# Kernel tuning notes

Measured on AMD Instinct MI355X. Metric: run time of the kernel, lower is better.

## Reference

```python
import jax, jax.numpy as jnp
import numpy as np

EPSILON_BASE = 0.1
N_ITERS = 10


def setup_inputs() -> dict:
    key = jax.random.key(0)
    k1, k2 = jax.random.split(key)
    N, D = 8192, 512
    embeddings = jax.random.normal(k1, (N, D), dtype=jnp.float32)
    target_noise = jax.random.normal(k2, (N, D), dtype=jnp.float32)
    return {"embeddings": embeddings, "target_noise": target_noise}


def _l2_normalize(x, axis=1, eps=1e-12):
    # matches torch.nn.functional.normalize (divide by max(norm, eps))
    norm = jnp.sqrt(jnp.sum(x * x, axis=axis, keepdims=True))
    return x / jnp.maximum(norm, eps)


def _sinkhorn(x, y):
    n, d = x.shape
    # normalize_embeddings=True path
    x = _l2_normalize(x, axis=1)
    y = _l2_normalize(y, axis=1)
    epsilon = EPSILON_BASE * 2.0
    # squared euclidean cost: C[i,j] = ||x_i - y_j||^2  (cdist p=2, squared)
    sq_x = jnp.sum(x * x, axis=1, keepdims=True)          # (n,1)
    sq_y = jnp.sum(y * y, axis=1, keepdims=True)          # (n,1)
    C = jnp.maximum(sq_x + sq_y.T - 2.0 * (x @ y.T), 0.0)  # (n,n)
    log_K = -C / epsilon

    def body(carry, _):
        log_u, log_v = carry
        log_u = -jax.nn.logsumexp(log_K + log_v[None, :], axis=1)
        log_v = -jax.nn.logsumexp(log_K.T + log_u[None, :], axis=1)
        return (log_u, log_v), None

    init = (jnp.zeros(n, dtype=x.dtype), jnp.zeros(n, dtype=y.dtype))
    (log_u, log_v), _ = jax.lax.scan(body, init, None, length=N_ITERS)

    log_P = log_u[:, None] + log_K + log_v[None, :]
    P = jnp.clip(jnp.exp(log_P), 0.0, 1.0)
    distance = jnp.sum(P * C) / n

    # nan/inf fallback: 1 - mean cosine similarity (x, y already unit norm)
    fallback = 1.0 - jnp.mean(jnp.sum(x * y, axis=1))
    bad = jnp.isnan(distance) | jnp.isinf(distance)
    return jnp.where(bad, fallback, distance)


def reference(embeddings, target_noise):
    if embeddings.ndim == 3:
        embeddings = embeddings.reshape(-1, embeddings.shape[-1])
        target_noise = target_noise.reshape(-1, target_noise.shape[-1])
    return _sinkhorn(embeddings, target_noise)
```

## Files before the change

kernel.cpp:

```cpp
#include <hip/hip_runtime.h>
#include <hip/hip_bf16.h>
#include <hip/hip_fp16.h>
#include <stdint.h>

#define NROW 8192
#define DIM  512
#define LN2   0.6931471805599453f
#define TEN_LOG2E 14.426950408889634f

typedef __attribute__((ext_vector_type(8))) short short8;
typedef __attribute__((ext_vector_type(4))) float f32x4;
typedef __attribute__((ext_vector_type(2))) float f32x2;

__device__ __forceinline__ float block_sum256(float v) {
  #pragma unroll
  for (int off = 32; off > 0; off >>= 1) v += __shfl_down(v, off, 64);
  __shared__ float sb[4];
  const int w = threadIdx.x >> 6;
  if ((threadIdx.x & 63) == 0) sb[w] = v;
  __syncthreads();
  return sb[0] + sb[1] + sb[2] + sb[3];
}

__global__ __launch_bounds__(256) void init_kernel(float* __restrict__ colrcp,
                                                   float* __restrict__ diagacc,
                                                   float* __restrict__ distacc) {
  const int g = blockIdx.x * 256 + threadIdx.x;
  colrcp[g] = 1.0f;
  if (g == 0) { diagacc[0] = 0.f; distacc[0] = 0.f; }
}

__global__ __launch_bounds__(256) void normalize_kernel(
    const float* __restrict__ X, const float* __restrict__ Y,
    __hip_bfloat16* __restrict__ Xn, __hip_bfloat16* __restrict__ Yn,
    float* __restrict__ diagacc) {
  const int wave = threadIdx.x >> 6, lane = threadIdx.x & 63;
  float dsum = 0.f;
  #pragma unroll
  for (int rr = 0; rr < 4; rr++) {
    const int row = blockIdx.x * 16 + wave * 4 + rr;
    const float4* xr = (const float4*)(X + (size_t)row * DIM);
    const float4* yr = (const float4*)(Y + (size_t)row * DIM);
    float4 x0 = xr[lane], x1 = xr[lane + 64];
    float4 y0 = yr[lane], y1 = yr[lane + 64];
    float sx = x0.x*x0.x + x0.y*x0.y + x0.z*x0.z + x0.w*x0.w
             + x1.x*x1.x + x1.y*x1.y + x1.z*x1.z + x1.w*x1.w;
    float sy = y0.x*y0.x + y0.y*y0.y + y0.z*y0.z + y0.w*y0.w
             + y1.x*y1.x + y1.y*y1.y + y1.z*y1.z + y1.w*y1.w;
    float sxy = x0.x*y0.x + x0.y*y0.y + x0.z*y0.z + x0.w*y0.w
              + x1.x*y1.x + x1.y*y1.y + x1.z*y1.z + x1.w*y1.w;
    #pragma unroll
    for (int off = 1; off < 64; off <<= 1) {
      sx  += __shfl_xor(sx, off, 64);
      sy  += __shfl_xor(sy, off, 64);
      sxy += __shfl_xor(sxy, off, 64);
    }
    const float rx = 1.0f / fmaxf(sqrtf(sx), 1e-12f);
    const float ry = 1.0f / fmaxf(sqrtf(sy), 1e-12f);
    if (lane == 0) dsum += sxy * rx * ry;
    ushort4 px, py;
    { __hip_bfloat16 b;
      b = __float2bfloat16(x0.x*rx); px.x = *(unsigned short*)&b;
      b = __float2bfloat16(x0.y*rx); px.y = *(unsigned short*)&b;
      b = __float2bfloat16(x0.z*rx); px.z = *(unsigned short*)&b;
      b = __float2bfloat16(x0.w*rx); px.w = *(unsigned short*)&b;
      b = __float2bfloat16(y0.x*ry); py.x = *(unsigned short*)&b;
      b = __float2bfloat16(y0.y*ry); py.y = *(unsigned short*)&b;
      b = __float2bfloat16(y0.z*ry); py.z = *(unsigned short*)&b;
      b = __float2bfloat16(y0.w*ry); py.w = *(unsigned short*)&b;
    }
    ((ushort4*)(Xn + (size_t)row * DIM))[lane] = px;
    ((ushort4*)(Yn + (size_t)row * DIM))[lane] = py;
    { __hip_bfloat16 b;
      b = __float2bfloat16(x1.x*rx); px.x = *(unsigned short*)&b;
      b = __float2bfloat16(x1.y*rx); px.y = *(unsigned short*)&b;
      b = __float2bfloat16(x1.z*rx); px.z = *(unsigned short*)&b;
      b = __float2bfloat16(x1.w*rx); px.w = *(unsigned short*)&b;
      b = __float2bfloat16(y1.x*ry); py.x = *(unsigned short*)&b;
      b = __float2bfloat16(y1.y*ry); py.y = *(unsigned short*)&b;
      b = __float2bfloat16(y1.z*ry); py.z = *(unsigned short*)&b;
      b = __float2bfloat16(y1.w*ry); py.w = *(unsigned short*)&b;
    }
    ((ushort4*)(Xn + (size_t)row * DIM))[lane + 64] = px;
    ((ushort4*)(Yn + (size_t)row * DIM))[lane + 64] = py;
  }
  if (lane == 0) atomicAdd(diagacc, dsum);
}

__global__ __launch_bounds__(256) void gemm_kernel(
    const __hip_bfloat16* __restrict__ A, const __hip_bfloat16* __restrict__ B,
    uint8_t* __restrict__ K, uint8_t* __restrict__ KT) {
  __shared__ short As[128 * 32];
  __shared__ short Bs[128 * 32];
  const int m0 = blockIdx.y * 128;
  const int n0 = blockIdx.x * 128;
  const int t = threadIdx.x;
  const int wave = t >> 6, lane = t & 63;
  const int wm = (wave & 1) * 64, wn = (wave >> 1) * 64;
  const int fr = lane & 15;
  const int fq = lane >> 4;

  f32x4 acc[4][4];
  #pragma unroll
  for (int i = 0; i < 4; i++)
    #pragma unroll
    for (int j = 0; j < 4; j++) acc[i][j] = (f32x4)0.f;

  const int L0 = t, L1 = t + 256;
  const int ar0 = L0 >> 2, ac0 = L0 & 3;
  const int ar1 = L1 >> 2, ac1 = L1 & 3;
  const int4* Ag = (const int4*)A;
  const int4* Bg = (const int4*)B;

  for (int kt = 0; kt < 16; ++kt) {
    const int kb = kt * 4;
    int4 a0 = Ag[(size_t)(m0 + ar0) * 64 + kb + ac0];
    int4 a1 = Ag[(size_t)(m0 + ar1) * 64 + kb + ac1];
    int4 b0 = Bg[(size_t)(n0 + ar0) * 64 + kb + ac0];
    int4 b1 = Bg[(size_t)(n0 + ar1) * 64 + kb + ac1];
    __syncthreads();
    ((int4*)As)[L0] = a0;
    ((int4*)As)[L1] = a1;
    ((int4*)Bs)[L0] = b0;
    ((int4*)Bs)[L1] = b1;
    __syncthreads();
    short8 af[4], bfr[4];
    #pragma unroll
    for (int i = 0; i < 4; i++) {
      af[i]  = *(const short8*)&As[(wm + i * 16 + fr) * 32 + fq * 8];
      bfr[i] = *(const short8*)&Bs[(wn + i * 16 + fr) * 32 + fq * 8];
    }
    #pragma unroll
    for (int i = 0; i < 4; i++)
      #pragma unroll
      for (int j = 0; j < 4; j++)
        acc[i][j] = __builtin_amdgcn_mfma_f32_16x16x32_bf16(af[i], bfr[j], acc[i][j], 0, 0, 0);
  }
  #pragma unroll
  for (int i = 0; i < 4; i++) {
    #pragma unroll
    for (int j = 0; j < 4; j++) {
      const int R  = wm + i * 16 + fq * 4;
      const int Cc = wn + j * 16 + fr;
      float v0 = exp2f(fminf(acc[i][j][0], 1.0f) * TEN_LOG2E);
      float v1 = exp2f(fminf(acc[i][j][1], 1.0f) * TEN_LOG2E);
      float v2 = exp2f(fminf(acc[i][j][2], 1.0f) * TEN_LOG2E);
      float v3 = exp2f(fminf(acc[i][j][3], 1.0f) * TEN_LOG2E);
      int pk = 0;
      pk = __builtin_amdgcn_cvt_pk_fp8_f32(v0, v1, pk, false);
      pk = __builtin_amdgcn_cvt_pk_fp8_f32(v2, v3, pk, true);
      *(int*)(KT + (size_t)(n0 + Cc) * NROW + m0 + R) = pk;
      uint8_t* kp = K + (size_t)(m0 + R) * NROW + n0 + Cc;
      kp[0]            = (uint8_t)(pk & 0xff);
      kp[NROW]         = (uint8_t)((pk >> 8) & 0xff);
      kp[2 * NROW]     = (uint8_t)((pk >> 16) & 0xff);
      kp[3 * NROW]     = (uint8_t)((pk >> 24) & 0xff);
    }
  }
}

__global__ __launch_bounds__(256) void pass_kernel(
    const uint8_t* __restrict__ M, const float* __restrict__ w,
    float* __restrict__ out) {
  __shared__ float4 wl[2048];
  const int t = threadIdx.x;
  #pragma unroll
  for (int c = 0; c < 8; c++) wl[c * 256 + t] = ((const float4*)w)[c * 256 + t];
  __syncthreads();
  const int wave = t >> 6, lane = t & 63;
  const int row = blockIdx.x * 4 + wave;
  const int4* Mr = (const int4*)(M + (size_t)row * NROW);
  int4 k[8];
  #pragma unroll
  for (int c = 0; c < 8; c++) k[c] = Mr[c * 64 + lane];
  float acc0 = 0.f, acc1 = 0.f;
  #pragma unroll
  for (int c = 0; c < 8; c++) {
    const int base = (c * 64 + lane) * 4;
    const int* kd = (const int*)&k[c];
    #pragma unroll
    for (int q = 0; q < 4; q++) {
      float4 ww = wl[base + q];
      f32x2 lo = __builtin_amdgcn_cvt_pk_f32_fp8(kd[q], false);
      f32x2 hi = __builtin_amdgcn_cvt_pk_f32_fp8(kd[q], true);
      acc0 += lo.x * ww.x + lo.y * ww.y;
      acc1 += hi.x * ww.z + hi.y * ww.w;
    }
  }
  float acc = acc0 + acc1;
  #pragma unroll
  for (int off = 32; off > 0; off >>= 1) acc += __shfl_down(acc, off, 64);
  if (lane == 0) out[row] = 1.0f / acc;
}

__global__ __launch_bounds__(256) void dist_kernel(
    const uint8_t* __restrict__ K, const float* __restrict__ v,
    const float* __restrict__ u, float* __restrict__ distacc) {
  __shared__ float4 wl[2048];
  const int t = threadIdx.x;
  #pragma unroll
  for (int c = 0; c < 8; c++) wl[c * 256 + t] = ((const float4*)v)[c * 256 + t];
  __syncthreads();
  const int wave = t >> 6, lane = t & 63;
  const int row = blockIdx.x * 4 + wave;
  const float ui = u[row];
  const int4* Kr = (const int4*)(K + (size_t)row * NROW);
  float acc = 0.f;
  #pragma unroll 2
  for (int c = 0; c < 8; c++) {
    int4 kq = Kr[c * 64 + lane];
    const int base = (c * 64 + lane) * 4;
    const int* kd = (const int*)&kq;
    #pragma unroll
    for (int q = 0; q < 4; q++) {
      float4 ww = wl[base + q];
      f32x2 lo = __builtin_amdgcn_cvt_pk_f32_fp8(kd[q], false);
      f32x2 hi = __builtin_amdgcn_cvt_pk_f32_fp8(kd[q], true);
      float kv[4] = {lo.x, lo.y, hi.x, hi.y};
      float wv[4] = {ww.x, ww.y, ww.z, ww.w};
      #pragma unroll
      for (int e = 0; e < 4; e++) {
        float p = fminf(ui * kv[e] * wv[e], 1.f);
        float cterm = 2.f - 0.2f * LN2 * __log2f(fmaxf(kv[e], 1e-6f));
        acc += p * cterm;
      }
    }
  }
  float tot = block_sum256(acc);
  if (t == 0) atomicAdd(distacc, tot);
}

__global__ void final_kernel(const float* __restrict__ distacc,
                             const float* __restrict__ diagacc,
                             float* __restrict__ out) {
  if (threadIdx.x == 0 && blockIdx.x == 0) {
    float d = distacc[0] * (1.0f / (float)NROW);
    float fb = 1.0f - diagacc[0] * (1.0f / (float)NROW);
    float v = (isnan(d) || isinf(d)) ? fb : d;
    __hip_bfloat16 b = __float2bfloat16(v);
    unsigned short h = *(unsigned short*)&b;
    ((unsigned int*)out)[0] = ((unsigned int)h << 16) | (unsigned int)h;
  }
}

extern "C" void kernel_launch(void* const* d_in, const int* in_sizes, int n_in,
                              void* d_out, int out_size, void* d_ws, size_t ws_size,
                              hipStream_t stream) {
  (void)in_sizes; (void)n_in; (void)out_size; (void)ws_size;
  const float* X = (const float*)d_in[0];
  const float* Y = (const float*)d_in[1];
  float* out = (float*)d_out;

  char* ws = (char*)d_ws;
  size_t off = 0;
  uint8_t* K  = (uint8_t*)(ws + off); off += (size_t)NROW * NROW;
  uint8_t* KT = (uint8_t*)(ws + off); off += (size_t)NROW * NROW;
  __hip_bfloat16* Xn = (__hip_bfloat16*)(ws + off); off += (size_t)NROW * DIM * 2;
  __hip_bfloat16* Yn = (__hip_bfloat16*)(ws + off); off += (size_t)NROW * DIM * 2;
  float* rowrcp  = (float*)(ws + off); off += NROW * 4;
  float* colrcp  = (float*)(ws + off); off += NROW * 4;
  float* diagacc = (float*)(ws + off); off += 256;
  float* distacc = (float*)(ws + off); off += 256;

  init_kernel<<<32, 256, 0, stream>>>(colrcp, diagacc, distacc);
  normalize_kernel<<<512, 256, 0, stream>>>(X, Y, Xn, Yn, diagacc);
  gemm_kernel<<<dim3(64, 64), 256, 0, stream>>>(Xn, Yn, K, KT);
  for (int it = 0; it < 10; ++it) {
    pass_kernel<<<2048, 256, 0, stream>>>(K,  colrcp, rowrcp);
    pass_kernel<<<2048, 256, 0, stream>>>(KT, rowrcp, colrcp);
  }
  dist_kernel<<<2048, 256, 0, stream>>>(K, colrcp, rowrcp, distacc);
  final_kernel<<<1, 64, 0, stream>>>(distacc, diagacc, out);
}
```

Before: 500.2 us.

## Fuse final column pass into distance kernel and restage GEMM transposed stores

The tenth column-scaling pass is folded into the distance kernel, which works over the transposed matrix. It computes v per row in registers and then sums P*C, so one full pass over the 64MB fp8 matrix is dropped. The GEMM epilogue now builds the row-major K tile through shared memory and writes it with coalesced 16-byte stores, replacing scattered byte stores. The LDS layouts for the GEMM operands and the weight vectors get XOR swizzles to avoid bank conflicts. The pass kernels also handle two rows per wave, so each LDS weight load feeds two rows.

Result: slower. 526.5 us (+5.3%).

```diff
diff --git a/kernel.cpp b/kernel.cpp
--- a/kernel.cpp
+++ b/kernel.cpp
@@ -1,6 +1,5 @@
 #include <hip/hip_runtime.h>
 #include <hip/hip_bf16.h>
-#include <hip/hip_fp16.h>
 #include <stdint.h>
 
 #define NROW 8192
@@ -12,21 +11,17 @@
 typedef __attribute__((ext_vector_type(4))) float f32x4;
 typedef __attribute__((ext_vector_type(2))) float f32x2;
 
-__device__ __forceinline__ float block_sum256(float v) {
-  #pragma unroll
-  for (int off = 32; off > 0; off >>= 1) v += __shfl_down(v, off, 64);
-  __shared__ float sb[4];
-  const int w = threadIdx.x >> 6;
-  if ((threadIdx.x & 63) == 0) sb[w] = v;
-  __syncthreads();
-  return sb[0] + sb[1] + sb[2] + sb[3];
-}
-
-__global__ __launch_bounds__(256) void init_kernel(float* __restrict__ colrcp,
+__device__ __forceinline__ float dot4fp8(int pk, float4 w) {
+  f32x2 lo = __builtin_amdgcn_cvt_pk_f32_fp8(pk, false);
+  f32x2 hi = __builtin_amdgcn_cvt_pk_f32_fp8(pk, true);
+  return lo.x * w.x + lo.y * w.y + hi.x * w.z + hi.y * w.w;
+}
+
+__global__ __launch_bounds__(256) void init_kernel(float* __restrict__ v,
                                                    float* __restrict__ diagacc,
                                                    float* __restrict__ distacc) {
   const int g = blockIdx.x * 256 + threadIdx.x;
-  colrcp[g] = 1.0f;
+  v[g] = 1.0f;
   if (g == 0) { diagacc[0] = 0.f; distacc[0] = 0.f; }
 }
 
@@ -89,9 +84,12 @@
 
 __global__ __launch_bounds__(256) void gemm_kernel(
     const __hip_bfloat16* __restrict__ A, const __hip_bfloat16* __restrict__ B,
-    uint8_t* __restrict__ K, uint8_t* __restrict__ KT) {
-  __shared__ short As[128 * 32];
-  __shared__ short Bs[128 * 32];
+    uint8_t* __restrict__ Kmat, uint8_t* __restrict__ T) {
+  __shared__ __align__(16) char smem[16896];
+  int4* As4 = (int4*)smem;
+  int4* Bs4 = (int4*)(smem + 8192);
+  int*  tileT = (int*)smem;
+
   const int m0 = blockIdx.y * 128;
   const int n0 = blockIdx.x * 128;
   const int t = threadIdx.x;
@@ -106,29 +104,31 @@
     #pragma unroll
     for (int j = 0; j < 4; j++) acc[i][j] = (f32x4)0.f;
 
-  const int L0 = t, L1 = t + 256;
-  const int ar0 = L0 >> 2, ac0 = L0 & 3;
-  const int ar1 = L1 >> 2, ac1 = L1 & 3;
+  const int r0 = t >> 2, c0 = t & 3;
+  const int ph = c0 ^ ((r0 >> 2) & 3);
+  const int dst0 = r0 * 4 + ph;
+  const int dst1 = (64 + r0) * 4 + ph;
+  const int pc = fq ^ ((fr >> 2) & 3);
   const int4* Ag = (const int4*)A;
   const int4* Bg = (const int4*)B;
 
   for (int kt = 0; kt < 16; ++kt) {
     const int kb = kt * 4;
-    int4 a0 = Ag[(size_t)(m0 + ar0) * 64 + kb + ac0];
-    int4 a1 = Ag[(size_t)(m0 + ar1) * 64 + kb + ac1];
-    int4 b0 = Bg[(size_t)(n0 + ar0) * 64 + kb + ac0];
-    int4 b1 = Bg[(size_t)(n0 + ar1) * 64 + kb + ac1];
+    int4 a0 = Ag[(size_t)(m0 + r0) * 64 + kb + c0];
+    int4 a1 = Ag[(size_t)(m0 + 64 + r0) * 64 + kb + c0];
+    int4 b0 = Bg[(size_t)(n0 + r0) * 64 + kb + c0];
+    int4 b1 = Bg[(size_t)(n0 + 64 + r0) * 64 + kb + c0];
     __syncthreads();
-    ((int4*)As)[L0] = a0;
-    ((int4*)As)[L1] = a1;
-    ((int4*)Bs)[L0] = b0;
-    ((int4*)Bs)[L1] = b1;
+    As4[dst0] = a0;
+    As4[dst1] = a1;
+    Bs4[dst0] = b0;
+    Bs4[dst1] = b1;
     __syncthreads();
     short8 af[4], bfr[4];
     #pragma unroll
     for (int i = 0; i < 4; i++) {
-      af[i]  = *(const short8*)&As[(wm + i * 16 + fr) * 32 + fq * 8];
-      bfr[i] = *(const short8*)&Bs[(wn + i * 16 + fr) * 32 + fq * 8];
+      af[i]  = *(const short8*)&As4[(wm + i * 16 + fr) * 4 + pc];
+      bfr[i] = *(const short8*)&Bs4[(wn + i * 16 + fr) * 4 + pc];
     }
     #pragma unroll
     for (int i = 0; i < 4; i++)
@@ -136,12 +136,15 @@
       for (int j = 0; j < 4; j++)
         acc[i][j] = __builtin_amdgcn_mfma_f32_16x16x32_bf16(af[i], bfr[j], acc[i][j], 0, 0, 0);
   }
-  #pragma unroll
-  for (int i = 0; i < 4; i++) {
-    #pragma unroll
-    for (int j = 0; j < 4; j++) {
+  __syncthreads();
+  #pragma unroll
+  for (int j = 0; j < 4; j++) {
+    const int Cc = wn + j * 16 + fr;
+    uint8_t* Trow = T + (size_t)(n0 + Cc) * NROW + m0;
+    #pragma unroll
+    for (int i = 0; i < 4; i++) {
       const int R  = wm + i * 16 + fq * 4;
-      const int Cc = wn + j * 16 + fr;
+      const int Rq = (wm >> 2) + i * 4 + fq;
       float v0 = exp2f(fminf(acc[i][j][0], 1.0f) * TEN_LOG2E);
       float v1 = exp2f(fminf(acc[i][j][1], 1.0f) * TEN_LOG2E);
       float v2 = exp2f(fminf(acc[i][j][2], 1.0f) * TEN_LOG2E);
@@ -149,85 +152,167 @@
       int pk = 0;
       pk = __builtin_amdgcn_cvt_pk_fp8_f32(v0, v1, pk, false);
       pk = __builtin_amdgcn_cvt_pk_fp8_f32(v2, v3, pk, true);
-      *(int*)(KT + (size_t)(n0 + Cc) * NROW + m0 + R) = pk;
-      uint8_t* kp = K + (size_t)(m0 + R) * NROW + n0 + Cc;
-      kp[0]            = (uint8_t)(pk & 0xff);
-      kp[NROW]         = (uint8_t)((pk >> 8) & 0xff);
-      kp[2 * NROW]     = (uint8_t)((pk >> 16) & 0xff);
-      kp[3 * NROW]     = (uint8_t)((pk >> 24) & 0xff);
-    }
-  }
-}
-
-__global__ __launch_bounds__(256) void pass_kernel(
+      *(int*)(Trow + R) = pk;
+      tileT[Rq * 132 + Cc] = pk;
+    }
+  }
+  __syncthreads();
+  const int rl = t >> 1;
+  const int half = t & 1;
+  const int rq = rl >> 2;
+  const int rb = (rl & 3) * 8;
+  uint8_t* Krow = Kmat + (size_t)(m0 + rl) * NROW + n0 + half * 64;
+  #pragma unroll
+  for (int q = 0; q < 4; q++) {
+    const int base = rq * 132 + half * 64 + q * 16;
+    int4 w0 = *(const int4*)&tileT[base];
+    int4 w1 = *(const int4*)&tileT[base + 4];
+    int4 w2 = *(const int4*)&tileT[base + 8];
+    int4 w3 = *(const int4*)&tileT[base + 12];
+    int outv[4];
+    const int* wp[4] = {(const int*)&w0, (const int*)&w1, (const int*)&w2, (const int*)&w3};
+    #pragma unroll
+    for (int d = 0; d < 4; d++) {
+      const unsigned a0 = ((unsigned)wp[d][0] >> rb) & 0xffu;
+      const unsigned a1 = ((unsigned)wp[d][1] >> rb) & 0xffu;
+      const unsigned a2 = ((unsigned)wp[d][2] >> rb) & 0xffu;
+      const unsigned a3 = ((unsigned)wp[d][3] >> rb) & 0xffu;
+      outv[d] = (int)(a0 | (a1 << 8) | (a2 << 16) | (a3 << 24));
+    }
+    int4 o; o.x = outv[0]; o.y = outv[1]; o.z = outv[2]; o.w = outv[3];
+    ((int4*)Krow)[q] = o;
+  }
+}
+
+__global__ __launch_bounds__(256) void rowpass_kernel(
     const uint8_t* __restrict__ M, const float* __restrict__ w,
     float* __restrict__ out) {
-  __shared__ float4 wl[2048];
+  __shared__ float wl[NROW];
+  float4* wl4 = (float4*)wl;
   const int t = threadIdx.x;
-  #pragma unroll
-  for (int c = 0; c < 8; c++) wl[c * 256 + t] = ((const float4*)w)[c * 256 + t];
+  {
+    const float4* wg = (const float4*)w;
+    #pragma unroll
+    for (int c = 0; c < 8; c++) {
+      int l = c * 256 + t;
+      int p = (l & ~3) | ((l & 3) ^ ((l >> 2) & 3));
+      wl4[p] = wg[l];
+    }
+  }
   __syncthreads();
   const int wave = t >> 6, lane = t & 63;
-  const int row = blockIdx.x * 4 + wave;
-  const int4* Mr = (const int4*)(M + (size_t)row * NROW);
-  int4 k[8];
-  #pragma unroll
-  for (int c = 0; c < 8; c++) k[c] = Mr[c * 64 + lane];
-  float acc0 = 0.f, acc1 = 0.f;
+  const int r0 = blockIdx.x * 8 + wave * 2;
+  const int4* row0 = (const int4*)(M + (size_t)r0 * NROW);
+  const int4* row1 = (const int4*)(M + (size_t)(r0 + 1) * NROW);
+  float d0 = 0.f, d1 = 0.f;
   #pragma unroll
   for (int c = 0; c < 8; c++) {
-    const int base = (c * 64 + lane) * 4;
-    const int* kd = (const int*)&k[c];
-    #pragma unroll
-    for (int q = 0; q < 4; q++) {
-      float4 ww = wl[base + q];
-      f32x2 lo = __builtin_amdgcn_cvt_pk_f32_fp8(kd[q], false);
-      f32x2 hi = __builtin_amdgcn_cvt_pk_f32_fp8(kd[q], true);
-      acc0 += lo.x * ww.x + lo.y * ww.y;
-      acc1 += hi.x * ww.z + hi.y * ww.w;
-    }
-  }
-  float acc = acc0 + acc1;
-  #pragma unroll
-  for (int off = 32; off > 0; off >>= 1) acc += __shfl_down(acc, off, 64);
-  if (lane == 0) out[row] = 1.0f / acc;
-}
-
-__global__ __launch_bounds__(256) void dist_kernel(
-    const uint8_t* __restrict__ K, const float* __restrict__ v,
-    const float* __restrict__ u, float* __restrict__ distacc) {
-  __shared__ float4 wl[2048];
+    const int idx = c * 64 + lane;
+    int4 k0 = row0[idx];
+    int4 k1 = row1[idx];
+    const int sw = idx & 3;
+    float4 w0 = wl4[idx * 4 + (0 ^ sw)];
+    float4 w1 = wl4[idx * 4 + (1 ^ sw)];
+    float4 w2 = wl4[idx * 4 + (2 ^ sw)];
+    float4 w3 = wl4[idx * 4 + (3 ^ sw)];
+    const int* p0 = (const int*)&k0;
+    const int* p1 = (const int*)&k1;
+    d0 += dot4fp8(p0[0], w0) + dot4fp8(p0[1], w1) + dot4fp8(p0[2], w2) + dot4fp8(p0[3], w3);
+    d1 += dot4fp8(p1[0], w0) + dot4fp8(p1[1], w1) + dot4fp8(p1[2], w2) + dot4fp8(p1[3], w3);
+  }
+  #pragma unroll
+  for (int off = 1; off < 64; off <<= 1) {
+    d0 += __shfl_xor(d0, off, 64);
+    d1 += __shfl_xor(d1, off, 64);
+  }
+  if (lane == 0) {
+    out[r0]     = 1.0f / d0;
+    out[r0 + 1] = 1.0f / d1;
+  }
+}
+
+__global__ __launch_bounds__(256) void vdist_kernel(
+    const uint8_t* __restrict__ T, const float* __restrict__ u,
+    float* __restrict__ distacc) {
+  __shared__ float wl[NROW];
+  float4* wl4 = (float4*)wl;
   const int t = threadIdx.x;
-  #pragma unroll
-  for (int c = 0; c < 8; c++) wl[c * 256 + t] = ((const float4*)v)[c * 256 + t];
+  {
+    const float4* wg = (const float4*)u;
+    #pragma unroll
+    for (int c = 0; c < 8; c++) {
+      int l = c * 256 + t;
+      int p = (l & ~3) | ((l & 3) ^ ((l >> 2) & 3));
+      wl4[p] = wg[l];
+    }
+  }
   __syncthreads();
   const int wave = t >> 6, lane = t & 63;
-  const int row = blockIdx.x * 4 + wave;
-  const float ui = u[row];
-  const int4* Kr = (const int4*)(K + (size_t)row * NROW);
+  const int r0 = blockIdx.x * 8 + wave * 2;
+  const int4* row0 = (const int4*)(T + (size_t)r0 * NROW);
+  const int4* row1 = (const int4*)(T + (size_t)(r0 + 1) * NROW);
+  float d0 = 0.f, d1 = 0.f;
+  #pragma unroll
+  for (int c = 0; c < 8; c++) {
+    const int idx = c * 64 + lane;
+    int4 k0 = row0[idx];
+    int4 k1 = row1[idx];
+    const int sw = idx & 3;
+    float4 w0 = wl4[idx * 4 + (0 ^ sw)];
+    float4 w1 = wl4[idx * 4 + (1 ^ sw)];
+    float4 w2 = wl4[idx * 4 + (2 ^ sw)];
+    float4 w3 = wl4[idx * 4 + (3 ^ sw)];
+    const int* p0 = (const int*)&k0;
+    const int* p1 = (const int*)&k1;
+    d0 += dot4fp8(p0[0], w0) + dot4fp8(p0[1], w1) + dot4fp8(p0[2], w2) + dot4fp8(p0[3], w3);
+    d1 += dot4fp8(p1[0], w0) + dot4fp8(p1[1], w1) + dot4fp8(p1[2], w2) + dot4fp8(p1[3], w3);
+  }
+  #pragma unroll
+  for (int off = 1; off < 64; off <<= 1) {
+    d0 += __shfl_xor(d0, off, 64);
+    d1 += __shfl_xor(d1, off, 64);
+  }
+  const float v0 = 1.0f / d0;
+  const float v1 = 1.0f / d1;
   float acc = 0.f;
   #pragma unroll 2
   for (int c = 0; c < 8; c++) {
-    int4 kq = Kr[c * 64 + lane];
-    const int base = (c * 64 + lane) * 4;
-    const int* kd = (const int*)&kq;
+    const int idx = c * 64 + lane;
+    int4 k0 = row0[idx];
+    int4 k1 = row1[idx];
+    const int sw = idx & 3;
+    float4 ww[4];
+    ww[0] = wl4[idx * 4 + (0 ^ sw)];
+    ww[1] = wl4[idx * 4 + (1 ^ sw)];
+    ww[2] = wl4[idx * 4 + (2 ^ sw)];
+    ww[3] = wl4[idx * 4 + (3 ^ sw)];
+    const int* p0 = (const int*)&k0;
+    const int* p1 = (const int*)&k1;
     #pragma unroll
     for (int q = 0; q < 4; q++) {
-      float4 ww = wl[base + q];
-      f32x2 lo = __builtin_amdgcn_cvt_pk_f32_fp8(kd[q], false);
-      f32x2 hi = __builtin_amdgcn_cvt_pk_f32_fp8(kd[q], true);
-      float kv[4] = {lo.x, lo.y, hi.x, hi.y};
-      float wv[4] = {ww.x, ww.y, ww.z, ww.w};
+      f32x2 lo0 = __builtin_amdgcn_cvt_pk_f32_fp8(p0[q], false);
+      f32x2 hi0 = __builtin_amdgcn_cvt_pk_f32_fp8(p0[q], true);
+      f32x2 lo1 = __builtin_amdgcn_cvt_pk_f32_fp8(p1[q], false);
+      f32x2 hi1 = __builtin_amdgcn_cvt_pk_f32_fp8(p1[q], true);
+      float kv0[4] = {lo0.x, lo0.y, hi0.x, hi0.y};
+      float kv1[4] = {lo1.x, lo1.y, hi1.x, hi1.y};
+      float uv[4] = {ww[q].x, ww[q].y, ww[q].z, ww[q].w};
       #pragma unroll
       for (int e = 0; e < 4; e++) {
-        float p = fminf(ui * kv[e] * wv[e], 1.f);
-        float cterm = 2.f - 0.2f * LN2 * __log2f(fmaxf(kv[e], 1e-6f));
-        acc += p * cterm;
+        float k0v = kv0[e], k1v = kv1[e];
+        float ct0 = 2.f - 0.2f * LN2 * __log2f(fmaxf(k0v, 1e-6f));
+        float ct1 = 2.f - 0.2f * LN2 * __log2f(fmaxf(k1v, 1e-6f));
+        acc += fminf(uv[e] * k0v * v0, 1.f) * ct0;
+        acc += fminf(uv[e] * k1v * v1, 1.f) * ct1;
       }
     }
   }
-  float tot = block_sum256(acc);
-  if (t == 0) atomicAdd(distacc, tot);
+  #pragma unroll
+  for (int off = 32; off > 0; off >>= 1) acc += __shfl_down(acc, off, 64);
+  __shared__ float sb[4];
+  if ((t & 63) == 0) sb[wave] = acc;
+  __syncthreads();
+  if (t == 0) atomicAdd(distacc, sb[0] + sb[1] + sb[2] + sb[3]);
 }
 
 __global__ void final_kernel(const float* __restrict__ distacc,
@@ -253,22 +338,23 @@
 
   char* ws = (char*)d_ws;
   size_t off = 0;
-  uint8_t* K  = (uint8_t*)(ws + off); off += (size_t)NROW * NROW;
-  uint8_t* KT = (uint8_t*)(ws + off); off += (size_t)NROW * NROW;
+  uint8_t* Kmat = (uint8_t*)(ws + off);             off += (size_t)NROW * NROW;
+  uint8_t* T    = (uint8_t*)(ws + off);             off += (size_t)NROW * NROW;
   __hip_bfloat16* Xn = (__hip_bfloat16*)(ws + off); off += (size_t)NROW * DIM * 2;
   __hip_bfloat16* Yn = (__hip_bfloat16*)(ws + off); off += (size_t)NROW * DIM * 2;
-  float* rowrcp  = (float*)(ws + off); off += NROW * 4;
-  float* colrcp  = (float*)(ws + off); off += NROW * 4;
+  float* uvec = (float*)(ws + off); off += NROW * 4;
+  float* vvec = (float*)(ws + off); off += NROW * 4;
   float* diagacc = (float*)(ws + off); off += 256;
   float* distacc = (float*)(ws + off); off += 256;
 
-  init_kernel<<<32, 256, 0, stream>>>(colrcp, diagacc, distacc);
+  init_kernel<<<32, 256, 0, stream>>>(vvec, diagacc, distacc);
   normalize_kernel<<<512, 256, 0, stream>>>(X, Y, Xn, Yn, diagacc);
-  gemm_kernel<<<dim3(64, 64), 256, 0, stream>>>(Xn, Yn, K, KT);
+  gemm_kernel<<<dim3(64, 64), 256, 0, stream>>>(Xn, Yn, Kmat, T);
   for (int it = 0; it < 10; ++it) {
-    pass_kernel<<<2048, 256, 0, stream>>>(K,  colrcp, rowrcp);
-    pass_kernel<<<2048, 256, 0, stream>>>(KT, rowrcp, colrcp);
-  }
-  dist_kernel<<<2048, 256, 0, stream>>>(K, colrcp, rowrcp, distacc);
+    rowpass_kernel<<<1024, 256, 0, stream>>>(Kmat, vvec, uvec);
+    if (it < 9)
+      rowpass_kernel<<<1024, 256, 0, stream>>>(T, uvec, vvec);
+  }
+  vdist_kernel<<<1024, 256, 0, stream>>>(T, uvec, distacc);
   final_kernel<<<1, 64, 0, stream>>>(distacc, diagacc, out);
 }
```
